# Kernel optimization log

Hardware: AMD Instinct MI355X
Metric: run time of the kernel (lower is better)

The kernel has to match this reference:

```python
import jax, jax.numpy as jnp
import numpy as np


def setup_inputs() -> dict:
    key = jax.random.key(0)
    k_x, k_B, k_C, k_D, k_step = jax.random.split(key, 5)
    Bsz, L, H = 8, 4096, 512
    P = 256  # effective state dim = dim_ssm_state // 2 (conj_sym)
    # s4d_inv init for Lambda (complex, stored as real/imag parts)
    n = jnp.arange(P, dtype=jnp.float32)
    Lambda_re = -0.5 * jnp.ones((P,), dtype=jnp.float32)
    Lambda_im = (P / np.pi) * (P / (2.0 * n + 1.0) - 1.0)
    # lecun_normal-ish init for B (P,H,2) and C (H,P,2), divided by sqrt(2)
    B = jax.random.normal(k_B, (P, H, 2), dtype=jnp.float32) * (1.0 / np.sqrt(H)) / np.sqrt(2.0)
    C = jax.random.normal(k_C, (H, P, 2), dtype=jnp.float32) * (1.0 / np.sqrt(P)) / np.sqrt(2.0)
    D = jax.random.normal(k_D, (H,), dtype=jnp.float32)
    dt_min, dt_max = 1e-3, 1e-1
    log_step = jax.random.uniform(k_step, (P,)) * (np.log(dt_max) - np.log(dt_min)) + np.log(dt_min)
    x = jax.random.normal(k_x, (Bsz, L, H), dtype=jnp.float32)
    return {"x": x, "Lambda_re": Lambda_re, "Lambda_im": Lambda_im,
            "B": B, "C": C, "D": D, "log_step": log_step.astype(jnp.float32)}


def _binary_op(q_i, q_j):
    A_i, b_i = q_i
    A_j, b_j = q_j
    return (A_j * A_i, A_j * b_i + b_j)


def reference(x, Lambda_re, Lambda_im, B, C, D, log_step):
    # Assemble complex params (conj_sym=True)
    Lam = Lambda_re + 1j * Lambda_im          # (P,)
    B_tilde = B[..., 0] + 1j * B[..., 1]      # (P,H)
    C_tilde = C[..., 0] + 1j * C[..., 1]      # (H,P)
    step = jnp.exp(log_step)                  # (P,) step_rescale = 1.0
    # ZOH discretization
    Lambda_bar = jnp.exp(Lam * step)                              # (P,)
    B_bar = ((Lambda_bar - 1.0) / Lam)[:, None] * B_tilde         # (P,H)
    # Bu elements: (Bsz, L, P) complex
    Bu = jnp.einsum('blh,ph->blp', x.astype(B_bar.dtype), B_bar)
    Lam_elems = jnp.broadcast_to(Lambda_bar, Bu.shape)
    # Parallel linear recurrence over time axis
    _, xs = jax.lax.associative_scan(_binary_op, (Lam_elems, Bu), axis=1)
    # Output projection with conjugate symmetry + D skip
    ys = 2.0 * jnp.einsum('blp,hp->blh', xs, C_tilde).real + D * x
    return ys
```

## Files before the change

kernel.cpp:

```cpp
#include <hip/hip_runtime.h>
#include <hip/hip_bf16.h>
#include <hip/hip_fp16.h>
#include <math.h>

#define BSZ 8
#define LSEQ 4096
#define HDIM 512
#define PDIM 256
#define MROWS (BSZ * LSEQ)
#define NDIM 512
#define CHUNK 32
#define NCHUNK (LSEQ / CHUNK)
#define LOG2CHUNK 5

typedef __attribute__((ext_vector_type(8))) short bf16x8;
typedef __attribute__((ext_vector_type(4))) float f32x4;

__device__ __forceinline__ void lambda_bar(const float* Lre, const float* Lim,
                                           const float* logstep, int p,
                                           float& ar, float& ai) {
    float step = expf(logstep[p]);
    float lr = Lre[p], li = Lim[p];
    float mag = expf(lr * step);
    ar = mag * cosf(li * step);
    ai = mag * sinf(li * step);
}

__global__ __launch_bounds__(256) void prep_w(
    const float* __restrict__ Lre, const float* __restrict__ Lim,
    const float* __restrict__ logstep,
    const float* __restrict__ Bmat, __hip_bfloat16* __restrict__ W1T,
    const float* __restrict__ Cmat, __hip_bfloat16* __restrict__ W2T) {
    const int bid = blockIdx.x;
    const int tid = threadIdx.x;
    if (bid < 512) {
        int idx = bid * 256 + tid;
        int p = idx >> 9, h = idx & 511;
        float ar, ai;
        lambda_bar(Lre, Lim, logstep, p, ar, ai);
        float lr = Lre[p], li = Lim[p];
        float den = lr * lr + li * li;
        float nr = ar - 1.0f, ni = ai;
        float fr = (nr * lr + ni * li) / den;
        float fi = (ni * lr - nr * li) / den;
        float br = Bmat[(size_t)(p * HDIM + h) * 2 + 0];
        float bi = Bmat[(size_t)(p * HDIM + h) * 2 + 1];
        W1T[(size_t)(2 * p) * HDIM + h]     = __float2bfloat16(fr * br - fi * bi);
        W1T[(size_t)(2 * p + 1) * HDIM + h] = __float2bfloat16(fr * bi + fi * br);
    } else {
        int idx = (bid - 512) * 256 + tid;
        int h = idx / PDIM, p = idx % PDIM;
        float cr = Cmat[(size_t)(h * PDIM + p) * 2 + 0];
        float ci = Cmat[(size_t)(h * PDIM + p) * 2 + 1];
        W2T[(size_t)h * NDIM + 2 * p]     = __float2bfloat16(2.0f * cr);
        W2T[(size_t)h * NDIM + 2 * p + 1] = __float2bfloat16(-2.0f * ci);
    }
}

__global__ __launch_bounds__(256) void gemm_xw(
    const float* __restrict__ A,
    const __hip_bfloat16* __restrict__ BT,
    __half* __restrict__ C,
    int M, int N, int K) {
    __shared__ __hip_bfloat16 smA[2 * 128 * 32];
    __shared__ __hip_bfloat16 smB[2 * 128 * 32];

    const int tid = threadIdx.x;
    const int lane = tid & 63;
    const int wave = tid >> 6;
    const int row0 = blockIdx.x * 128;
    const int col0 = blockIdx.y * 128;
    const int wm = (wave >> 1) * 64;
    const int wn = (wave & 1) * 64;

    const int sr = lane >> 2;
    const int swz_st = ((lane >> 2) & 3) ^ ((lane >> 4) & 3);
    const int sk = (((lane & 3) ^ swz_st) * 8);
    const int quad = lane >> 4;
    const int l15 = lane & 15;
    const int rq = ((quad ^ ((l15 & 3) ^ ((l15 >> 2) & 3))) * 8);

    f32x4 acc[4][4] = {};

    auto stageB = [&](int buf, int t) {
        const int k0 = t << 5;
#pragma unroll
        for (int q = 0; q < 2; ++q) {
            const int chunk = wave * 32 + q * 16;
            const __hip_bfloat16* gB = BT + (size_t)(col0 + chunk + sr) * K + k0 + sk;
            __builtin_amdgcn_global_load_lds(
                (const __attribute__((address_space(1))) void*)gB,
                (__attribute__((address_space(3))) void*)&smB[buf * 4096 + chunk * 32],
                16, 0, 0);
        }
    };
    auto loadA = [&](int t, float4* ar) {
        const int k0 = t << 5;
#pragma unroll
        for (int q = 0; q < 2; ++q) {
            const float* gA = A + (size_t)(row0 + wave * 32 + q * 16 + sr) * K + k0 + sk;
            ar[q * 2]     = *(const float4*)gA;
            ar[q * 2 + 1] = *(const float4*)(gA + 4);
        }
    };
    auto writeA = [&](int buf, const float4* ar) {
#pragma unroll
        for (int q = 0; q < 2; ++q) {
            union { bf16x8 v; __hip_bfloat16 h[8]; } o;
            o.h[0] = __float2bfloat16(ar[q * 2].x);
            o.h[1] = __float2bfloat16(ar[q * 2].y);
            o.h[2] = __float2bfloat16(ar[q * 2].z);
            o.h[3] = __float2bfloat16(ar[q * 2].w);
            o.h[4] = __float2bfloat16(ar[q * 2 + 1].x);
            o.h[5] = __float2bfloat16(ar[q * 2 + 1].y);
            o.h[6] = __float2bfloat16(ar[q * 2 + 1].z);
            o.h[7] = __float2bfloat16(ar[q * 2 + 1].w);
            *(bf16x8*)&smA[buf * 4096 + (wave * 32 + q * 16 + sr) * 32 + (lane & 3) * 8] = o.v;
        }
    };

    const int nk = K >> 5;
    float4 ar[4];
    loadA(0, ar);
    stageB(0, 0);
    writeA(0, ar);
    __syncthreads();

    int buf = 0;
    for (int t = 0; t < nk; ++t) {
        if (t + 1 < nk) {
            loadA(t + 1, ar);
            stageB(buf ^ 1, t + 1);
        }

        const __hip_bfloat16* sA = &smA[buf * 4096];
        const __hip_bfloat16* sB = &smB[buf * 4096];
        bf16x8 af[4], bfr[4];
#pragma unroll
        for (int i = 0; i < 4; ++i)
            af[i] = *(const bf16x8*)&sA[(wm + i * 16 + l15) * 32 + rq];
#pragma unroll
        for (int j = 0; j < 4; ++j)
            bfr[j] = *(const bf16x8*)&sB[(wn + j * 16 + l15) * 32 + rq];
#pragma unroll
        for (int i = 0; i < 4; ++i)
#pragma unroll
            for (int j = 0; j < 4; ++j)
                acc[i][j] = __builtin_amdgcn_mfma_f32_16x16x32_bf16(
                    af[i], bfr[j], acc[i][j], 0, 0, 0);

        if (t + 1 < nk) writeA(buf ^ 1, ar);
        __syncthreads();
        buf ^= 1;
    }

#pragma unroll
    for (int i = 0; i < 4; ++i) {
        const int mbase = row0 + wm + i * 16 + quad * 4;
#pragma unroll
        for (int j = 0; j < 4; ++j) {
            const int col = col0 + wn + j * 16 + l15;
#pragma unroll
            for (int r = 0; r < 4; ++r) {
                const size_t m = (size_t)(mbase + r);
                C[m * N + col] = __half(acc[i][j][r]);
            }
        }
    }
}

__global__ __launch_bounds__(256) void gemm_bt_skip(
    const __hip_bfloat16* __restrict__ A,
    const __hip_bfloat16* __restrict__ BT,
    float* __restrict__ C,
    const float* __restrict__ Dvec,
    const float* __restrict__ Xskip,
    int M, int N, int K) {
    __shared__ __hip_bfloat16 smA[3 * 128 * 32];
    __shared__ __hip_bfloat16 smB[3 * 128 * 32];

    const int tid = threadIdx.x;
    const int lane = tid & 63;
    const int wave = tid >> 6;
    const int row0 = blockIdx.x * 128;
    const int col0 = blockIdx.y * 128;
    const int wm = (wave >> 1) * 64;
    const int wn = (wave & 1) * 64;

    const int sr = lane >> 2;
    const int swz_st = ((lane >> 2) & 3) ^ ((lane >> 4) & 3);
    const int sk = (((lane & 3) ^ swz_st) * 8);
    const int quad = lane >> 4;
    const int l15 = lane & 15;
    const int rq = ((quad ^ ((l15 & 3) ^ ((l15 >> 2) & 3))) * 8);

    f32x4 acc[4][4] = {};

    auto stage = [&](int buf, int t) {
        const int k0 = t << 5;
#pragma unroll
        for (int q = 0; q < 2; ++q) {
            const int chunk = wave * 32 + q * 16;
            const __hip_bfloat16* gA = A + (size_t)(row0 + chunk + sr) * K + k0 + sk;
            __builtin_amdgcn_global_load_lds(
                (const __attribute__((address_space(1))) void*)gA,
                (__attribute__((address_space(3))) void*)&smA[buf * 4096 + chunk * 32],
                16, 0, 0);
            const __hip_bfloat16* gB = BT + (size_t)(col0 + chunk + sr) * K + k0 + sk;
            __builtin_amdgcn_global_load_lds(
                (const __attribute__((address_space(1))) void*)gB,
                (__attribute__((address_space(3))) void*)&smB[buf * 4096 + chunk * 32],
                16, 0, 0);
        }
    };

    const int nk = K >> 5;
    stage(0, 0);
    stage(1, 1);
    asm volatile("s_waitcnt vmcnt(4)" ::: "memory");
    __builtin_amdgcn_s_barrier();

    int cur = 0;
    for (int t = 0; t < nk; ++t) {
        if (t + 2 < nk) {
            int st = cur + 2; if (st >= 3) st -= 3;
            stage(st, t + 2);
        }

        const __hip_bfloat16* sA = &smA[cur * 4096];
        const __hip_bfloat16* sB = &smB[cur * 4096];
        bf16x8 af[4], bfr[4];
#pragma unroll
        for (int i = 0; i < 4; ++i)
            af[i] = *(const bf16x8*)&sA[(wm + i * 16 + l15) * 32 + rq];
#pragma unroll
        for (int j = 0; j < 4; ++j)
            bfr[j] = *(const bf16x8*)&sB[(wn + j * 16 + l15) * 32 + rq];
#pragma unroll
        for (int i = 0; i < 4; ++i)
#pragma unroll
            for (int j = 0; j < 4; ++j)
                acc[i][j] = __builtin_amdgcn_mfma_f32_16x16x32_bf16(
                    af[i], bfr[j], acc[i][j], 0, 0, 0);

        if (t + 1 < nk) {
            if (t + 2 < nk)
                asm volatile("s_waitcnt vmcnt(4)" ::: "memory");
            else
                asm volatile("s_waitcnt vmcnt(0)" ::: "memory");
            __builtin_amdgcn_s_barrier();
        }
        cur += 1; if (cur == 3) cur = 0;
    }

#pragma unroll
    for (int i = 0; i < 4; ++i) {
        const int mbase = row0 + wm + i * 16 + quad * 4;
#pragma unroll
        for (int j = 0; j < 4; ++j) {
            const int col = col0 + wn + j * 16 + l15;
            const float dv = Dvec[col];
#pragma unroll
            for (int r = 0; r < 4; ++r) {
                const size_t m = (size_t)(mbase + r);
                C[m * N + col] = acc[i][j][r] + dv * Xskip[m * N + col];
            }
        }
    }
}

__global__ __launch_bounds__(256) void scan_chunks(
    const __half2* __restrict__ Bu2,
    const float* __restrict__ Lre, const float* __restrict__ Lim,
    const float* __restrict__ logstep,
    float2* __restrict__ S) {
    int b = blockIdx.x / NCHUNK;
    int c = blockIdx.x % NCHUNK;
    int p = threadIdx.x;
    float ar, ai;
    lambda_bar(Lre, Lim, logstep, p, ar, ai);
    float sr = 0.0f, si = 0.0f;
    size_t m0 = (size_t)b * LSEQ + (size_t)c * CHUNK;
    for (int j = 0; j < CHUNK; ++j) {
        float2 u = __half22float2(Bu2[(m0 + j) * PDIM + p]);
        float nsr = ar * sr - ai * si + u.x;
        float nsi = ar * si + ai * sr + u.y;
        sr = nsr; si = nsi;
    }
    S[(size_t)(b * NCHUNK + c) * PDIM + p] = make_float2(sr, si);
}

__global__ __launch_bounds__(256) void scan_carry(
    const float2* __restrict__ S,
    const float* __restrict__ Lre, const float* __restrict__ Lim,
    const float* __restrict__ logstep,
    float2* __restrict__ carry) {
    const int wid = blockIdx.x * 4 + (threadIdx.x >> 6);
    const int b = wid >> 8;
    const int p = wid & 255;
    const int lane = threadIdx.x & 63;
    const int c0 = 2 * lane, c1 = 2 * lane + 1;
    float alr, ali;
    lambda_bar(Lre, Lim, logstep, p, alr, ali);
#pragma unroll
    for (int i = 0; i < LOG2CHUNK; ++i) {
        float tr = alr * alr - ali * ali;
        float ti = 2.0f * alr * ali;
        alr = tr; ali = ti;
    }
    float2 s0 = S[(size_t)(b * NCHUNK + c0) * PDIM + p];
    float2 s1 = S[(size_t)(b * NCHUNK + c1) * PDIM + p];
    float Ar = alr * alr - ali * ali;
    float Ai = 2.0f * alr * ali;
    float br = alr * s0.x - ali * s0.y + s1.x;
    float bi = alr * s0.y + ali * s0.x + s1.y;
#pragma unroll
    for (int d = 1; d < 64; d <<= 1) {
        float pAr = __shfl_up(Ar, d);
        float pAi = __shfl_up(Ai, d);
        float pbr = __shfl_up(br, d);
        float pbi = __shfl_up(bi, d);
        if (lane >= d) {
            float nAr = Ar * pAr - Ai * pAi;
            float nAi = Ar * pAi + Ai * pAr;
            float nbr = Ar * pbr - Ai * pbi + br;
            float nbi = Ar * pbi + Ai * pbr + bi;
            Ar = nAr; Ai = nAi; br = nbr; bi = nbi;
        }
    }
    float er = __shfl_up(br, 1);
    float ei = __shfl_up(bi, 1);
    if (lane == 0) { er = 0.0f; ei = 0.0f; }
    carry[(size_t)(b * NCHUNK + c0) * PDIM + p] = make_float2(er, ei);
    carry[(size_t)(b * NCHUNK + c1) * PDIM + p] =
        make_float2(alr * er - ali * ei + s0.x, alr * ei + ali * er + s0.y);
}

__global__ __launch_bounds__(256) void scan_apply(
    const __half2* __restrict__ Bu2,
    const float* __restrict__ Lre, const float* __restrict__ Lim,
    const float* __restrict__ logstep,
    const float2* __restrict__ carry,
    ushort2* __restrict__ xsb2) {
    int b = blockIdx.x / NCHUNK;
    int c = blockIdx.x % NCHUNK;
    int p = threadIdx.x;
    float ar, ai;
    lambda_bar(Lre, Lim, logstep, p, ar, ai);
    float2 c0 = carry[(size_t)(b * NCHUNK + c) * PDIM + p];
    float sr = c0.x, si = c0.y;
    size_t m0 = (size_t)b * LSEQ + (size_t)c * CHUNK;
    for (int j = 0; j < CHUNK; ++j) {
        size_t idx = (m0 + j) * PDIM + p;
        float2 u = __half22float2(Bu2[idx]);
        float nsr = ar * sr - ai * si + u.x;
        float nsi = ar * si + ai * sr + u.y;
        sr = nsr; si = nsi;
        union { ushort2 u2; __hip_bfloat16 h[2]; } o;
        o.h[0] = __float2bfloat16(sr);
        o.h[1] = __float2bfloat16(si);
        xsb2[idx] = o.u2;
    }
}

extern "C" void kernel_launch(void* const* d_in, const int* in_sizes, int n_in,
                              void* d_out, int out_size, void* d_ws, size_t ws_size,
                              hipStream_t stream) {
    const float* x       = (const float*)d_in[0];
    const float* Lre     = (const float*)d_in[1];
    const float* Lim     = (const float*)d_in[2];
    const float* Bmat    = (const float*)d_in[3];
    const float* Cmat    = (const float*)d_in[4];
    const float* Dvec    = (const float*)d_in[5];
    const float* logstep = (const float*)d_in[6];
    float* out = (float*)d_out;

    char* ws = (char*)d_ws;
    const size_t MB = 1u << 20;
    __hip_bfloat16* xsb = (__hip_bfloat16*)(ws + 0);
    __half* Bu          = (__half*)(ws + 32 * MB);
    __hip_bfloat16* W1T = (__hip_bfloat16*)(ws + 64 * MB);
    __hip_bfloat16* W2T = (__hip_bfloat16*)(ws + 64 * MB + 512 * 1024);
    float2* S     = (float2*)(ws + 66 * MB);
    float2* carry = (float2*)(ws + 68 * MB);

    prep_w<<<1024, 256, 0, stream>>>(Lre, Lim, logstep, Bmat, W1T, Cmat, W2T);

    dim3 ggrid(MROWS / 128, NDIM / 128);
    gemm_xw<<<ggrid, 256, 0, stream>>>(x, W1T, Bu, MROWS, NDIM, HDIM);

    scan_chunks<<<BSZ * NCHUNK, 256, 0, stream>>>((const __half2*)Bu,
                                                  Lre, Lim, logstep, S);
    scan_carry<<<BSZ * PDIM / 4, 256, 0, stream>>>(S, Lre, Lim, logstep, carry);
    scan_apply<<<BSZ * NCHUNK, 256, 0, stream>>>((const __half2*)Bu,
                                                 Lre, Lim, logstep, carry,
                                                 (ushort2*)xsb);

    dim3 ggrid2(MROWS / 128, HDIM / 128);
    gemm_bt_skip<<<ggrid2, 256, 0, stream>>>(
        xsb, W2T, out, Dvec, x, MROWS, HDIM, NDIM);
}
```

Baseline: 213.6 us.

## Deepen gemm_xw prefetch to two stages with triple-buffered B and manual waitcnts

Changes the first GEMM's main loop from single-stage to two-stage prefetch. A uses two register sets and B a third shared-memory buffer, and __syncthreads is replaced by explicit vmcnt/lgkmcnt waits plus s_barrier. The goal is to hide global load latency behind MFMA work. It costs more registers and LDS, and correctness depends on the hand-set vmcnt(6) count matching the number of outstanding loads.

New measurement: 293.3 us. +37.3%, slower.

```diff
diff --git a/kernel.cpp b/kernel.cpp
--- a/kernel.cpp
+++ b/kernel.cpp
@@ -63,7 +63,7 @@
     __half* __restrict__ C,
     int M, int N, int K) {
     __shared__ __hip_bfloat16 smA[2 * 128 * 32];
-    __shared__ __hip_bfloat16 smB[2 * 128 * 32];
+    __shared__ __hip_bfloat16 smB[3 * 128 * 32];
 
     const int tid = threadIdx.x;
     const int lane = tid & 63;
@@ -120,21 +120,27 @@
     };
 
     const int nk = K >> 5;
-    float4 ar[4];
-    loadA(0, ar);
+    float4 arr[2][4];
+
+    loadA(0, arr[0]);
     stageB(0, 0);
-    writeA(0, ar);
-    __syncthreads();
-
-    int buf = 0;
+    loadA(1, arr[1]);
+    stageB(1, 1);
+    asm volatile("s_waitcnt vmcnt(6)" ::: "memory");
+    writeA(0, arr[0]);
+    asm volatile("s_waitcnt lgkmcnt(0)" ::: "memory");
+    __builtin_amdgcn_s_barrier();
+
+    int curB = 0;
     for (int t = 0; t < nk; ++t) {
-        if (t + 1 < nk) {
-            loadA(t + 1, ar);
-            stageB(buf ^ 1, t + 1);
-        }
-
-        const __hip_bfloat16* sA = &smA[buf * 4096];
-        const __hip_bfloat16* sB = &smB[buf * 4096];
+        if (t + 2 < nk) {
+            int sb = curB + 2; if (sb >= 3) sb -= 3;
+            loadA(t + 2, arr[t & 1]);
+            stageB(sb, t + 2);
+        }
+
+        const __hip_bfloat16* sA = &smA[(t & 1) * 4096];
+        const __hip_bfloat16* sB = &smB[curB * 4096];
         bf16x8 af[4], bfr[4];
 #pragma unroll
         for (int i = 0; i < 4; ++i)
@@ -149,9 +155,16 @@
                 acc[i][j] = __builtin_amdgcn_mfma_f32_16x16x32_bf16(
                     af[i], bfr[j], acc[i][j], 0, 0, 0);
 
-        if (t + 1 < nk) writeA(buf ^ 1, ar);
-        __syncthreads();
-        buf ^= 1;
+        if (t + 1 < nk) {
+            if (t + 2 < nk)
+                asm volatile("s_waitcnt vmcnt(6)" ::: "memory");
+            else
+                asm volatile("s_waitcnt vmcnt(0)" ::: "memory");
+            writeA((t + 1) & 1, arr[(t + 1) & 1]);
+            asm volatile("s_waitcnt lgkmcnt(0)" ::: "memory");
+            __builtin_amdgcn_s_barrier();
+        }
+        curB += 1; if (curB == 3) curB = 0;
     }
 
 #pragma unroll
```
